# Performance work log

Measured on AMD Instinct MI355X. Metric: run time of the kernel, lower is better.

The kernel has to match this reference:

```python
import jax, jax.numpy as jnp
import numpy as np

B, T, F, H = 64, 2048, 256, 256


def setup_inputs() -> dict:
    key = jax.random.key(0)
    k1, k2, k3 = jax.random.split(key, 3)
    return {
        "carry": jnp.zeros((B, H), jnp.float32),
        "x": jax.random.normal(k1, (B, T, F), jnp.float32),
        "Wi": jax.random.normal(k2, (F, 3 * H), jnp.float32) * (1.0 / np.sqrt(F)),
        "Wh": jax.random.normal(k3, (H, 3 * H), jnp.float32) * (1.0 / np.sqrt(H)),
        "bh": jnp.zeros((3 * H,), jnp.float32),
    }


def reference(carry, x, Wi, Wh, bh):
    # time_major=False: transpose to [T, B, F] for the scan
    xt = jnp.transpose(x, (1, 0, 2))
    # Precompute all input projections in one big GEMM (same math as per-step
    # dense_i since inputs don't depend on the carry): [T, B, 3H]
    xi = jnp.einsum("tbf,fg->tbg", xt, Wi)

    def step(h, xi_t):
        hp = h @ Wh + bh  # recurrent projections (bias on hidden side, as in flax GRUCell)
        i_r, i_z, i_n = jnp.split(xi_t, 3, axis=-1)
        h_r, h_z, h_n = jnp.split(hp, 3, axis=-1)
        r = jax.nn.sigmoid(i_r + h_r)
        z = jax.nn.sigmoid(i_z + h_z)
        n = jnp.tanh(i_n + r * h_n)
        new_h = (1.0 - z) * n + z * h
        return new_h, new_h

    carry, hidden = jax.lax.scan(step, carry, xi, unroll=1)
    hidden = jnp.transpose(hidden, (1, 0, 2))  # back to [B, T, H]
    return carry, hidden
```

## Files before the change

### kernel.cpp

```cpp
#include <hip/hip_runtime.h>
#include <hip/hip_bf16.h>
#include <stdint.h>
#include <math.h>

#define NB   64
#define NT   2048
#define NF   256
#define NH   256
#define NG   768

typedef unsigned int u32;
typedef _Float16 f16;
typedef f16 half2v __attribute__((ext_vector_type(2)));

__device__ __forceinline__ u32 packpair(float a, float b) {
    return __builtin_bit_cast(u32, __builtin_amdgcn_cvt_pkrtz(a, b));
}

__device__ __forceinline__ float fdot2u(u32 w, u32 h, float acc) {
#if __has_builtin(__builtin_amdgcn_fdot2)
    return __builtin_amdgcn_fdot2(__builtin_bit_cast(half2v, w),
                                  __builtin_bit_cast(half2v, h), acc, false);
#else
    half2v wv = __builtin_bit_cast(half2v, w), hv = __builtin_bit_cast(half2v, h);
    return fmaf((float)wv[1], (float)hv[1], fmaf((float)wv[0], (float)hv[0], acc));
#endif
}

__device__ __forceinline__ float quad_sum(float v) {
    int i = __builtin_bit_cast(int, v);
    v += __builtin_bit_cast(float, __builtin_amdgcn_update_dpp(0, i, 0xB1, 0xF, 0xF, true));
    i = __builtin_bit_cast(int, v);
    v += __builtin_bit_cast(float, __builtin_amdgcn_update_dpp(0, i, 0x4E, 0xF, 0xF, true));
    return v;
}

__global__ __launch_bounds__(256, 2) void xi_gemm(const float* __restrict__ x,
                                                  const float* __restrict__ Wi,
                                                  f16* __restrict__ xi) {
    __shared__ u32 xs2[32][128];
    const int tid = threadIdx.x;
    const int r0  = blockIdx.x * 32;
    {
        const int hi = tid >> 7, lo = tid & 127;
        #pragma unroll
        for (int rr = 0; rr < 16; ++rr) {
            const int r = rr * 2 + hi;
            const float2 v = *(const float2*)&x[(size_t)(r0 + r) * NF + lo * 2];
            xs2[r][lo] = packpair(v.x, v.y);
        }
    }
    __syncthreads();

    float acc[32][3];
    #pragma unroll
    for (int r = 0; r < 32; ++r) { acc[r][0] = 0.f; acc[r][1] = 0.f; acc[r][2] = 0.f; }

    for (int kp2 = 0; kp2 < 64; ++kp2) {
        const int k = kp2 * 4;
        u32 wA[3], wB[3];
        #pragma unroll
        for (int j = 0; j < 3; ++j) {
            const float* wp = &Wi[(size_t)k * NG + j * 256 + tid];
            wA[j] = packpair(wp[0],              wp[NG]);
            wB[j] = packpair(wp[2 * (size_t)NG], wp[3 * (size_t)NG]);
        }
        #pragma unroll
        for (int r = 0; r < 32; ++r) {
            const uint2 xv = *(const uint2*)&xs2[r][kp2 * 2];
            #pragma unroll
            for (int j = 0; j < 3; ++j)
                acc[r][j] = fdot2u(wB[j], xv.y, fdot2u(wA[j], xv.x, acc[r][j]));
        }
    }

    #pragma unroll
    for (int r = 0; r < 32; ++r)
        #pragma unroll
        for (int j = 0; j < 3; ++j)
            xi[(size_t)(r0 + r) * NG + j * 256 + tid] = (f16)acc[r][j];
}

__global__ __launch_bounds__(768) void gru_rec(
        const float* __restrict__ carry,
        const f16*   __restrict__ xi,
        const float* __restrict__ Wh,
        const float* __restrict__ bh,
        float* __restrict__ out_carry,
        float* __restrict__ out_hidden) {
    __shared__ u32   hsh2[4][132];
    __shared__ float hp_lds[NG];
    __shared__ float bsh[NG];

    const int tid  = threadIdx.x;
    const int b    = blockIdx.x;
    const int c    = tid >> 2;
    const int kc   = tid & 3;
    const int col0 = c * 4;
    const int k0   = kc * 64;

    u32 wh2[128];
    #pragma unroll
    for (int j = 0; j < 4; ++j)
        #pragma unroll
        for (int p = 0; p < 32; ++p) {
            const float* wp = &Wh[(size_t)(k0 + 2 * p) * NG + col0 + j];
            wh2[j * 32 + p] = packpair(wp[0], wp[NG]);
        }

    if (tid < NG) bsh[tid] = bh[tid];
    float hreg = 0.f;
    if (tid < NH) {
        hreg = carry[(size_t)b * NH + tid];
        const f16 hf = (f16)hreg;
        #pragma unroll
        for (int rc = 0; rc < 4; ++rc) ((f16*)&hsh2[rc][0])[tid] = hf;
    }
    __syncthreads();

    const f16* xb = xi + (size_t)b * NT * NG;
    float x0 = 0.f, x1 = 0.f, x2 = 0.f, y0 = 0.f, y1 = 0.f, y2 = 0.f;
    if (tid < NH) {
        x0 = (float)xb[tid];      x1 = (float)xb[256 + tid];      x2 = (float)xb[512 + tid];
        y0 = (float)xb[NG + tid]; y1 = (float)xb[NG + 256 + tid]; y2 = (float)xb[NG + 512 + tid];
    }

#define GRU_STEP(T, X0, X1, X2)                                                   \
    {                                                                             \
        float n0 = 0.f, n1 = 0.f, n2 = 0.f;                                       \
        if (tid < NH && (T) + 2 < NT) {                                           \
            const f16* xp = xb + (size_t)((T) + 2) * NG + tid;                    \
            n0 = (float)xp[0]; n1 = (float)xp[256]; n2 = (float)xp[512];          \
        }                                                                         \
        float a0 = 0.f, a1 = 0.f, a2 = 0.f, a3 = 0.f;                             \
        const uint4* hp4 = (const uint4*)&hsh2[kc][kc * 32];                      \
        _Pragma("unroll")                                                         \
        for (int p4 = 0; p4 < 8; ++p4) {                                          \
            const uint4 hv = hp4[p4];                                             \
            a0 = fdot2u(wh2[  0 + p4 * 4 + 0], hv.x, a0);                         \
            a1 = fdot2u(wh2[ 32 + p4 * 4 + 0], hv.x, a1);                         \
            a2 = fdot2u(wh2[ 64 + p4 * 4 + 0], hv.x, a2);                         \
            a3 = fdot2u(wh2[ 96 + p4 * 4 + 0], hv.x, a3);                         \
            a0 = fdot2u(wh2[  0 + p4 * 4 + 1], hv.y, a0);                         \
            a1 = fdot2u(wh2[ 32 + p4 * 4 + 1], hv.y, a1);                         \
            a2 = fdot2u(wh2[ 64 + p4 * 4 + 1], hv.y, a2);                         \
            a3 = fdot2u(wh2[ 96 + p4 * 4 + 1], hv.y, a3);                         \
            a0 = fdot2u(wh2[  0 + p4 * 4 + 2], hv.z, a0);                         \
            a1 = fdot2u(wh2[ 32 + p4 * 4 + 2], hv.z, a1);                         \
            a2 = fdot2u(wh2[ 64 + p4 * 4 + 2], hv.z, a2);                         \
            a3 = fdot2u(wh2[ 96 + p4 * 4 + 2], hv.z, a3);                         \
            a0 = fdot2u(wh2[  0 + p4 * 4 + 3], hv.w, a0);                         \
            a1 = fdot2u(wh2[ 32 + p4 * 4 + 3], hv.w, a1);                         \
            a2 = fdot2u(wh2[ 64 + p4 * 4 + 3], hv.w, a2);                         \
            a3 = fdot2u(wh2[ 96 + p4 * 4 + 3], hv.w, a3);                         \
        }                                                                         \
        a0 = quad_sum(a0); a1 = quad_sum(a1); a2 = quad_sum(a2); a3 = quad_sum(a3); \
        if (kc == 0) {                                                            \
            float4 hpv; hpv.x = a0; hpv.y = a1; hpv.z = a2; hpv.w = a3;           \
            *(float4*)&hp_lds[col0] = hpv;                                        \
        }                                                                         \
        __syncthreads();                                                          \
        if (tid < NH) {                                                           \
            const float hpr = hp_lds[tid]       + bsh[tid];                       \
            const float hpz = hp_lds[256 + tid] + bsh[256 + tid];                 \
            const float hpn = hp_lds[512 + tid] + bsh[512 + tid];                 \
            const float rg  = 1.f / (1.f + __expf(-((X0) + hpr)));                \
            const float zg  = 1.f / (1.f + __expf(-((X1) + hpz)));                \
            const float tt  = (X2) + rg * hpn;                                    \
            const float ng  = 1.f - 2.f / (__expf(2.f * tt) + 1.f);               \
            const float hn  = (1.f - zg) * ng + zg * hreg;                        \
            hreg = hn;                                                            \
            out_hidden[((size_t)b * NT + (T)) * NH + tid] = hn;                   \
            const f16 hf = (f16)hn;                                               \
            _Pragma("unroll")                                                     \
            for (int rc = 0; rc < 4; ++rc) ((f16*)&hsh2[rc][0])[tid] = hf;        \
        }                                                                         \
        __syncthreads();                                                          \
        X0 = n0; X1 = n1; X2 = n2;                                                \
    }

    for (int t = 0; t < NT; t += 2) {
        GRU_STEP(t,     x0, x1, x2);
        GRU_STEP(t + 1, y0, y1, y2);
    }
#undef GRU_STEP

    if (tid < NH) out_carry[(size_t)b * NH + tid] = hreg;
}

extern "C" void kernel_launch(void* const* d_in, const int* in_sizes, int n_in,
                              void* d_out, int out_size, void* d_ws, size_t ws_size,
                              hipStream_t stream) {
    const float* carry = (const float*)d_in[0];
    const float* x     = (const float*)d_in[1];
    const float* Wi    = (const float*)d_in[2];
    const float* Wh    = (const float*)d_in[3];
    const float* bh    = (const float*)d_in[4];

    float* out_carry  = (float*)d_out;
    float* out_hidden = out_carry + (size_t)NB * NH;

    f16* xi = (f16*)d_ws;

    xi_gemm<<<dim3(NB * NT / 32), dim3(256), 0, stream>>>(x, Wi, xi);
    gru_rec<<<dim3(NB), dim3(768), 0, stream>>>(carry, xi, Wh, bh,
                                                out_carry, out_hidden);
}
```

Measured before the change: 3.067 ms.

## Use packed fp16 FMA accumulation and one-barrier double-buffered GRU step

```diff
diff --git a/kernel.cpp b/kernel.cpp
--- a/kernel.cpp
+++ b/kernel.cpp
@@ -1,7 +1,6 @@
 #include <hip/hip_runtime.h>
-#include <hip/hip_bf16.h>
+#include <hip/hip_fp16.h>
 #include <stdint.h>
-#include <math.h>
 
 #define NB   64
 #define NT   2048
@@ -10,23 +9,20 @@
 #define NG   768
 
 typedef unsigned int u32;
-typedef _Float16 f16;
-typedef f16 half2v __attribute__((ext_vector_type(2)));
 
 __device__ __forceinline__ u32 packpair(float a, float b) {
     return __builtin_bit_cast(u32, __builtin_amdgcn_cvt_pkrtz(a, b));
 }
-
-__device__ __forceinline__ float fdot2u(u32 w, u32 h, float acc) {
-#if __has_builtin(__builtin_amdgcn_fdot2)
-    return __builtin_amdgcn_fdot2(__builtin_bit_cast(half2v, w),
-                                  __builtin_bit_cast(half2v, h), acc, false);
-#else
-    half2v wv = __builtin_bit_cast(half2v, w), hv = __builtin_bit_cast(half2v, h);
-    return fmaf((float)wv[1], (float)hv[1], fmaf((float)wv[0], (float)hv[0], acc));
-#endif
+__device__ __forceinline__ u32 hfma2u(u32 w, u32 h, u32 acc) {
+    __half2 r = __hfma2(__builtin_bit_cast(__half2, w),
+                        __builtin_bit_cast(__half2, h),
+                        __builtin_bit_cast(__half2, acc));
+    return __builtin_bit_cast(u32, r);
 }
-
+__device__ __forceinline__ float pairsum(u32 a) {
+    __half2 h = __builtin_bit_cast(__half2, a);
+    return __low2float(h) + __high2float(h);
+}
 __device__ __forceinline__ float quad_sum(float v) {
     int i = __builtin_bit_cast(int, v);
     v += __builtin_bit_cast(float, __builtin_amdgcn_update_dpp(0, i, 0xB1, 0xF, 0xF, true));
@@ -37,7 +33,7 @@
 
 __global__ __launch_bounds__(256, 2) void xi_gemm(const float* __restrict__ x,
                                                   const float* __restrict__ Wi,
-                                                  f16* __restrict__ xi) {
+                                                  __half* __restrict__ xi) {
     __shared__ u32 xs2[32][128];
     const int tid = threadIdx.x;
     const int r0  = blockIdx.x * 32;
@@ -52,9 +48,9 @@
     }
     __syncthreads();
 
-    float acc[32][3];
+    u32 acc2[32][3];
     #pragma unroll
-    for (int r = 0; r < 32; ++r) { acc[r][0] = 0.f; acc[r][1] = 0.f; acc[r][2] = 0.f; }
+    for (int r = 0; r < 32; ++r) { acc2[r][0] = 0; acc2[r][1] = 0; acc2[r][2] = 0; }
 
     for (int kp2 = 0; kp2 < 64; ++kp2) {
         const int k = kp2 * 4;
@@ -70,7 +66,7 @@
             const uint2 xv = *(const uint2*)&xs2[r][kp2 * 2];
             #pragma unroll
             for (int j = 0; j < 3; ++j)
-                acc[r][j] = fdot2u(wB[j], xv.y, fdot2u(wA[j], xv.x, acc[r][j]));
+                acc2[r][j] = hfma2u(wB[j], xv.y, hfma2u(wA[j], xv.x, acc2[r][j]));
         }
     }
 
@@ -78,114 +74,86 @@
     for (int r = 0; r < 32; ++r)
         #pragma unroll
         for (int j = 0; j < 3; ++j)
-            xi[(size_t)(r0 + r) * NG + j * 256 + tid] = (f16)acc[r][j];
+            xi[(size_t)(r0 + r) * NG + j * 256 + tid] = __float2half(pairsum(acc2[r][j]));
 }
 
-__global__ __launch_bounds__(768) void gru_rec(
+__global__ __launch_bounds__(1024, 1) void gru_rec(
         const float* __restrict__ carry,
-        const f16*   __restrict__ xi,
+        const __half* __restrict__ xi,
         const float* __restrict__ Wh,
         const float* __restrict__ bh,
         float* __restrict__ out_carry,
         float* __restrict__ out_hidden) {
-    __shared__ u32   hsh2[4][132];
-    __shared__ float hp_lds[NG];
-    __shared__ float bsh[NG];
+    __shared__ u32 hsh[2][4][136];
 
-    const int tid  = threadIdx.x;
-    const int b    = blockIdx.x;
-    const int c    = tid >> 2;
-    const int kc   = tid & 3;
-    const int col0 = c * 4;
-    const int k0   = kc * 64;
+    const int tid = threadIdx.x;
+    const int b   = blockIdx.x;
+    const int u   = tid >> 2;
+    const int kc  = tid & 3;
+    const int k0  = kc * 64;
 
-    u32 wh2[128];
+    u32 wh2[3][32];
     #pragma unroll
-    for (int j = 0; j < 4; ++j)
+    for (int j = 0; j < 3; ++j) {
+        const float* wp = &Wh[(size_t)k0 * NG + j * 256 + u];
         #pragma unroll
         for (int p = 0; p < 32; ++p) {
-            const float* wp = &Wh[(size_t)(k0 + 2 * p) * NG + col0 + j];
-            wh2[j * 32 + p] = packpair(wp[0], wp[NG]);
+            wh2[j][p] = packpair(wp[0], wp[NG]);
+            wp += 2 * (size_t)NG;
         }
+    }
+    const float br = bh[u], bz = bh[256 + u], bn = bh[512 + u];
 
-    if (tid < NG) bsh[tid] = bh[tid];
-    float hreg = 0.f;
-    if (tid < NH) {
-        hreg = carry[(size_t)b * NH + tid];
-        const f16 hf = (f16)hreg;
-        #pragma unroll
-        for (int rc = 0; rc < 4; ++rc) ((f16*)&hsh2[rc][0])[tid] = hf;
-    }
+    float hreg = carry[(size_t)b * NH + u];
+    ((__half*)&hsh[0][kc][0])[u] = __float2half(hreg);
+
+    const __half* xp = xi + (size_t)b * NT * NG;
+    __half xr = xp[u], xz = xp[256 + u], xn = xp[512 + u];
+    const __half* xq = xp + NG;
+    float* op = out_hidden + (size_t)b * NT * NH + u;
+
     __syncthreads();
 
-    const f16* xb = xi + (size_t)b * NT * NG;
-    float x0 = 0.f, x1 = 0.f, x2 = 0.f, y0 = 0.f, y1 = 0.f, y2 = 0.f;
-    if (tid < NH) {
-        x0 = (float)xb[tid];      x1 = (float)xb[256 + tid];      x2 = (float)xb[512 + tid];
-        y0 = (float)xb[NG + tid]; y1 = (float)xb[NG + 256 + tid]; y2 = (float)xb[NG + 512 + tid];
+#define FMA3(p, hc) { a0 = hfma2u(wh2[0][p], hc, a0); \
+                      a1 = hfma2u(wh2[1][p], hc, a1); \
+                      a2 = hfma2u(wh2[2][p], hc, a2); }
+
+    for (int t = 0; t < NT; ++t) {
+        const uint4* hp4 = (const uint4*)&hsh[t & 1][kc][kc * 32];
+        u32 a0 = 0, a1 = 0, a2 = 0;
+        #pragma unroll
+        for (int ph = 0; ph < 4; ++ph) {
+            const uint4 h0 = hp4[2 * ph], h1 = hp4[2 * ph + 1];
+            FMA3(8 * ph + 0, h0.x); FMA3(8 * ph + 1, h0.y);
+            FMA3(8 * ph + 2, h0.z); FMA3(8 * ph + 3, h0.w);
+            FMA3(8 * ph + 4, h1.x); FMA3(8 * ph + 5, h1.y);
+            FMA3(8 * ph + 6, h1.z); FMA3(8 * ph + 7, h1.w);
+            asm volatile("" ::: "memory");
+        }
+        float s0 = quad_sum(pairsum(a0));
+        float s1 = quad_sum(pairsum(a1));
+        float s2 = quad_sum(pairsum(a2));
+
+        const float rg = 1.f / (1.f + __expf(-(__half2float(xr) + s0 + br)));
+        const float zg = 1.f / (1.f + __expf(-(__half2float(xz) + s1 + bz)));
+        const float tt = __half2float(xn) + rg * (s2 + bn);
+        const float ng = 1.f - 2.f / (__expf(2.f * tt) + 1.f);
+        const float hn = (1.f - zg) * ng + zg * hreg;
+        hreg = hn;
+
+        if (kc == 0) *op = hn;
+        op += NH;
+        ((__half*)&hsh[(t + 1) & 1][kc][0])[u] = __float2half(hn);
+
+        if (t + 1 < NT) {
+            xr = xq[u]; xz = xq[256 + u]; xn = xq[512 + u];
+            xq += NG;
+        }
+        __syncthreads();
     }
+#undef FMA3
 
-#define GRU_STEP(T, X0, X1, X2)                                                   \
-    {                                                                             \
-        float n0 = 0.f, n1 = 0.f, n2 = 0.f;                                       \
-        if (tid < NH && (T) + 2 < NT) {                                           \
-            const f16* xp = xb + (size_t)((T) + 2) * NG + tid;                    \
-            n0 = (float)xp[0]; n1 = (float)xp[256]; n2 = (float)xp[512];          \
-        }                                                                         \
-        float a0 = 0.f, a1 = 0.f, a2 = 0.f, a3 = 0.f;                             \
-        const uint4* hp4 = (const uint4*)&hsh2[kc][kc * 32];                      \
-        _Pragma("unroll")                                                         \
-        for (int p4 = 0; p4 < 8; ++p4) {                                          \
-            const uint4 hv = hp4[p4];                                             \
-            a0 = fdot2u(wh2[  0 + p4 * 4 + 0], hv.x, a0);                         \
-            a1 = fdot2u(wh2[ 32 + p4 * 4 + 0], hv.x, a1);                         \
-            a2 = fdot2u(wh2[ 64 + p4 * 4 + 0], hv.x, a2);                         \
-            a3 = fdot2u(wh2[ 96 + p4 * 4 + 0], hv.x, a3);                         \
-            a0 = fdot2u(wh2[  0 + p4 * 4 + 1], hv.y, a0);                         \
-            a1 = fdot2u(wh2[ 32 + p4 * 4 + 1], hv.y, a1);                         \
-            a2 = fdot2u(wh2[ 64 + p4 * 4 + 1], hv.y, a2);                         \
-            a3 = fdot2u(wh2[ 96 + p4 * 4 + 1], hv.y, a3);                         \
-            a0 = fdot2u(wh2[  0 + p4 * 4 + 2], hv.z, a0);                         \
-            a1 = fdot2u(wh2[ 32 + p4 * 4 + 2], hv.z, a1);                         \
-            a2 = fdot2u(wh2[ 64 + p4 * 4 + 2], hv.z, a2);                         \
-            a3 = fdot2u(wh2[ 96 + p4 * 4 + 2], hv.z, a3);                         \
-            a0 = fdot2u(wh2[  0 + p4 * 4 + 3], hv.w, a0);                         \
-            a1 = fdot2u(wh2[ 32 + p4 * 4 + 3], hv.w, a1);                         \
-            a2 = fdot2u(wh2[ 64 + p4 * 4 + 3], hv.w, a2);                         \
-            a3 = fdot2u(wh2[ 96 + p4 * 4 + 3], hv.w, a3);                         \
-        }                                                                         \
-        a0 = quad_sum(a0); a1 = quad_sum(a1); a2 = quad_sum(a2); a3 = quad_sum(a3); \
-        if (kc == 0) {                                                            \
-            float4 hpv; hpv.x = a0; hpv.y = a1; hpv.z = a2; hpv.w = a3;           \
-            *(float4*)&hp_lds[col0] = hpv;                                        \
-        }                                                                         \
-        __syncthreads();                                                          \
-        if (tid < NH) {                                                           \
-            const float hpr = hp_lds[tid]       + bsh[tid];                       \
-            const float hpz = hp_lds[256 + tid] + bsh[256 + tid];                 \
-            const float hpn = hp_lds[512 + tid] + bsh[512 + tid];                 \
-            const float rg  = 1.f / (1.f + __expf(-((X0) + hpr)));                \
-            const float zg  = 1.f / (1.f + __expf(-((X1) + hpz)));                \
-            const float tt  = (X2) + rg * hpn;                                    \
-            const float ng  = 1.f - 2.f / (__expf(2.f * tt) + 1.f);               \
-            const float hn  = (1.f - zg) * ng + zg * hreg;                        \
-            hreg = hn;                                                            \
-            out_hidden[((size_t)b * NT + (T)) * NH + tid] = hn;                   \
-            const f16 hf = (f16)hn;                                               \
-            _Pragma("unroll")                                                     \
-            for (int rc = 0; rc < 4; ++rc) ((f16*)&hsh2[rc][0])[tid] = hf;        \
-        }                                                                         \
-        __syncthreads();                                                          \
-        X0 = n0; X1 = n1; X2 = n2;                                                \
-    }
-
-    for (int t = 0; t < NT; t += 2) {
-        GRU_STEP(t,     x0, x1, x2);
-        GRU_STEP(t + 1, y0, y1, y2);
-    }
-#undef GRU_STEP
-
-    if (tid < NH) out_carry[(size_t)b * NH + tid] = hreg;
+    if (kc == 0) out_carry[(size_t)b * NH + u] = hreg;
 }
 
 extern "C" void kernel_launch(void* const* d_in, const int* in_sizes, int n_in,
@@ -200,9 +168,9 @@
     float* out_carry  = (float*)d_out;
     float* out_hidden = out_carry + (size_t)NB * NH;
 
-    f16* xi = (f16*)d_ws;
+    __half* xi = (__half*)d_ws;
 
     xi_gemm<<<dim3(NB * NT / 32), dim3(256), 0, stream>>>(x, Wi, xi);
-    gru_rec<<<dim3(NB), dim3(768), 0, stream>>>(carry, xi, Wh, bh,
-                                                out_carry, out_hidden);
+    gru_rec<<<dim3(NB), dim3(1024), 0, stream>>>(carry, xi, Wh, bh,
+                                                 out_carry, out_hidden);
 }
```

Result: slower. 3.618 ms (+18.0%).
